# Optimization experiments

Measured on AMD Instinct MI355X. Metric: run time of the kernel, lower is better.

Reference implementation:

```python
import jax, jax.numpy as jnp
import numpy as np

GROUPS = 1024
K_N = 32
FEAT_DIM = 64
EPS = 1e-05


def farthest_point_sample(xyz, npoint):
    # xyz: [B, N, 3] -> centroids [B, npoint] int32
    # Original torch code starts from a random point; we use index 0 for determinism.
    B, N, _ = xyz.shape

    def step(carry, _):
        distance, farthest = carry
        centroid = jnp.take_along_axis(xyz, farthest[:, None, None], axis=1)  # [B,1,3]
        dist = jnp.sum((xyz - centroid) ** 2, axis=-1)  # [B,N]
        distance = jnp.minimum(distance, dist)
        new_far = jnp.argmax(distance, axis=-1).astype(jnp.int32)
        return (distance, new_far), farthest

    init = (jnp.full((B, N), 1e10, dtype=xyz.dtype), jnp.zeros((B,), jnp.int32))
    _, cents = jax.lax.scan(step, init, None, length=npoint)
    return cents.T  # [B, npoint]


def index_points(points, idx):
    # points: [B, N, C]; idx: [B, ...] -> [B, ..., C]
    B = points.shape[0]
    bidx = jnp.arange(B).reshape((B,) + (1,) * (idx.ndim - 1))
    return points[bidx, idx]


def square_distance(src, dst):
    # src [B,S,C], dst [B,N,C] -> [B,S,N]
    d = -2.0 * jnp.einsum('bsc,bnc->bsn', src, dst)
    d = d + jnp.sum(src ** 2, -1)[:, :, None]
    d = d + jnp.sum(dst ** 2, -1)[:, None, :]
    return d


def setup_inputs() -> dict:
    key = jax.random.key(0)
    k1, k2 = jax.random.split(key)
    xyz = jax.random.normal(k1, (8, 3, 4096), dtype=jnp.float32)
    feats = jax.random.normal(k2, (8, FEAT_DIM, 4096), dtype=jnp.float32)
    affine_alpha_p = jnp.ones((1, 1, 1, FEAT_DIM), jnp.float32)
    affine_beta_p = jnp.zeros((1, 1, 1, FEAT_DIM), jnp.float32)
    return {"xyz": xyz, "feats": feats,
            "affine_alpha_p": affine_alpha_p, "affine_beta_p": affine_beta_p}


def reference(xyz, feats, affine_alpha_p, affine_beta_p):
    xyz = jnp.transpose(xyz, (0, 2, 1))      # [B,N,3]
    feats = jnp.transpose(feats, (0, 2, 1))  # [B,N,D]
    B, N, _ = xyz.shape
    S, k = GROUPS, K_N

    fps_idx = farthest_point_sample(xyz, S)          # [B,S]
    new_xyz = index_points(xyz, fps_idx)             # [B,S,3]
    new_feats = index_points(feats, fps_idx)         # [B,S,D]

    sqr = square_distance(new_xyz, xyz)              # [B,S,N]
    _, idx = jax.lax.top_k(-sqr, k)                  # smallest-k -> [B,S,k]
    grouped = index_points(feats, idx)               # [B,S,k,D]

    mean = new_feats[:, :, None, :]                  # [B,S,1,D]
    diff = grouped - mean
    # torch.std over flattened per-batch, unbiased (ddof=1)
    std = jnp.std(diff.reshape(B, -1), axis=-1, ddof=1)[:, None, None, None]
    grouped = diff / (std + EPS)
    grouped = affine_alpha_p * grouped + affine_beta_p

    point_feats = jnp.concatenate(
        [grouped, grouped - new_feats[:, :, None, :]], axis=-1)  # [B,S,k,2D]

    new_feats_out = jnp.transpose(new_feats, (0, 2, 1))          # [B,D,S]
    new_xyz_out = jnp.transpose(new_xyz, (0, 2, 1))              # [B,3,S]
    point_feats_out = jnp.transpose(point_feats, (0, 3, 1, 2))   # [B,2D,S,k]
    return (new_xyz_out, new_feats_out, point_feats_out)
```

## Files before the change

kernel.cpp:

```cpp
#include <hip/hip_runtime.h>

#define NPTS 4096
#define NSAMP 1024
#define KNN_K 32
#define FDIM 64
#define EPSF 1e-5f

typedef float v2f __attribute__((ext_vector_type(2)));

#define DPP_FMAX(CTRL)                                                           \
  {                                                                              \
    int _o = __builtin_amdgcn_update_dpp(0, __float_as_int(wv), CTRL, 0xf, 0xf,  \
                                         true);                                  \
    wv = fmaxf(wv, __int_as_float(_o));                                          \
  }

#define DPP_MAX64(CTRL)                                                          \
  {                                                                              \
    unsigned _olo = (unsigned)__builtin_amdgcn_update_dpp(0, (int)klo, CTRL,     \
                                                          0xf, 0xf, true);       \
    unsigned _ohi = (unsigned)__builtin_amdgcn_update_dpp(0, (int)khi, CTRL,     \
                                                          0xf, 0xf, true);       \
    unsigned long long _ok = ((unsigned long long)_ohi << 32) | _olo;            \
    unsigned long long _ck = ((unsigned long long)khi << 32) | klo;              \
    if (_ok > _ck) { klo = _olo; khi = _ohi; }                                   \
  }

__global__ __launch_bounds__(512) void fps_kernel(const float* __restrict__ xyz,
                                                  int* __restrict__ fps_idx,
                                                  float* __restrict__ sqnorm) {
#pragma clang fp contract(off)
  __shared__ float4 pts[NPTS];
  __shared__ unsigned long long skeys[2][8];
  __shared__ int fpsb[NSAMP];
  const int b = blockIdx.x, t = threadIdx.x;
  const int lane = t & 63, w = t >> 6;
  const float* xb = xyz + (size_t)b * 3 * NPTS;
  v2f px[4], py[4], pz[4];
  float dist[8];
#pragma unroll
  for (int j = 0; j < 4; ++j) {
    int p0 = (2 * j) * 512 + t, p1 = (2 * j + 1) * 512 + t;
    float x0 = xb[p0], y0 = xb[NPTS + p0], z0 = xb[2 * NPTS + p0];
    float x1 = xb[p1], y1 = xb[NPTS + p1], z1 = xb[2 * NPTS + p1];
    float sq0 = __fadd_rn(__fadd_rn(__fmul_rn(x0, x0), __fmul_rn(y0, y0)),
                          __fmul_rn(z0, z0));
    float sq1 = __fadd_rn(__fadd_rn(__fmul_rn(x1, x1), __fmul_rn(y1, y1)),
                          __fmul_rn(z1, z1));
    pts[p0] = make_float4(x0, y0, z0, sq0);
    pts[p1] = make_float4(x1, y1, z1, sq1);
    sqnorm[b * NPTS + p0] = sq0;
    sqnorm[b * NPTS + p1] = sq1;
    px[j].x = x0; px[j].y = x1;
    py[j].x = y0; py[j].y = y1;
    pz[j].x = z0; pz[j].y = z1;
    dist[2 * j] = 1e10f;
    dist[2 * j + 1] = 1e10f;
  }
  if (t == 0) fpsb[0] = 0;
  __syncthreads();
  float4 c = pts[0];
  for (int it = 1; it < NSAMP; ++it) {
    v2f vcx, vcy, vcz;
    vcx.x = c.x; vcx.y = c.x;
    vcy.x = c.y; vcy.y = c.y;
    vcz.x = c.z; vcz.y = c.z;
#pragma unroll
    for (int j = 0; j < 4; ++j) {
      v2f dx = px[j] - vcx;
      v2f dy = py[j] - vcy;
      v2f dz = pz[j] - vcz;
      v2f dd = (dx * dx + dy * dy) + dz * dz;
      dist[2 * j] = fminf(dist[2 * j], dd.x);
      dist[2 * j + 1] = fminf(dist[2 * j + 1], dd.y);
    }
    float m0 = fmaxf(dist[0], dist[1]), m1 = fmaxf(dist[2], dist[3]);
    float m2 = fmaxf(dist[4], dist[5]), m3 = fmaxf(dist[6], dist[7]);
    float wv = fmaxf(fmaxf(m0, m1), fmaxf(m2, m3));
    DPP_FMAX(0x111)
    DPP_FMAX(0x112)
    DPP_FMAX(0x114)
    DPP_FMAX(0x118)
    DPP_FMAX(0x142)
    DPP_FMAX(0x143)
    unsigned wvb = (unsigned)__builtin_amdgcn_readlane(__float_as_int(wv), 63);
    float wvf = __uint_as_float(wvb);
    int kk = 0, found = 0;
    unsigned long long mm = 0ull;
#pragma unroll
    for (int k = 0; k < 8; ++k) {
      unsigned long long m = __ballot(dist[k] == wvf);
      if (!found && m != 0ull) { kk = k; mm = m; found = 1; }
    }
    int fl = __ffsll(mm) - 1;
    unsigned idx = (unsigned)(kk * 512 + (w << 6) + fl);
    unsigned klo = (wvb << 12) | (4095u - idx);
    unsigned khi = wvb >> 20;
    const int buf = it & 1;
    if (lane == 63) skeys[buf][w] = ((unsigned long long)khi << 32) | klo;
    __syncthreads();
    unsigned long long kk2 = skeys[buf][lane & 7];
    klo = (unsigned)kk2;
    khi = (unsigned)(kk2 >> 32);
    DPP_MAX64(0x111)
    DPP_MAX64(0x112)
    DPP_MAX64(0x114)
    unsigned flo = (unsigned)__builtin_amdgcn_readlane((int)klo, 7);
    int far = 4095 - (int)(flo & 0xfffu);
    if (t == 0) fpsb[it] = far;
    c = pts[far];
  }
  __syncthreads();
#pragma unroll
  for (int k = 0; k < 2; ++k)
    fps_idx[b * NSAMP + k * 512 + t] = fpsb[k * 512 + t];
}

__global__ __launch_bounds__(256) void gather_feats_kernel(const float* __restrict__ feats,
                                                           const int* __restrict__ fps,
                                                           float* __restrict__ out1,
                                                           float* __restrict__ nf) {
  int i = blockIdx.x * 256 + threadIdx.x;
  int s = i & 1023, c = (i >> 10) & 63, b = i >> 16;
  int p = fps[(b << 10) + s];
  float v = feats[((size_t)(b * 64 + c)) * NPTS + p];
  out1[(b * 64 + c) * 1024 + s] = v;
  nf[(((b << 10) + s) << 6) + c] = v;
}

__global__ __launch_bounds__(256) void gather_xyz_kernel(const float* __restrict__ xyz,
                                                         const float* __restrict__ sqnorm,
                                                         const int* __restrict__ fps,
                                                         float* __restrict__ out0,
                                                         float4* __restrict__ nx4) {
  int i = blockIdx.x * 256 + threadIdx.x;
  int b = i >> 10, s = i & 1023;
  int p = fps[i];
  const float* xb = xyz + (size_t)b * 3 * NPTS;
  float x = xb[p], y = xb[NPTS + p], z = xb[2 * NPTS + p];
  nx4[i] = make_float4(x, y, z, sqnorm[b * NPTS + p]);
  out0[(b * 3 + 0) * 1024 + s] = x;
  out0[(b * 3 + 1) * 1024 + s] = y;
  out0[(b * 3 + 2) * 1024 + s] = z;
}

__device__ __forceinline__ unsigned long long mk_key(float xn, float yn, float zn,
                                                     float sq, float cx, float cy,
                                                     float cz, float src2, int n) {
  float dot = __fmaf_rn(zn, cz, __fmaf_rn(yn, cy, __fmul_rn(xn, cx)));
  float d = __fadd_rn(__fadd_rn(__fmul_rn(-2.0f, dot), src2), sq);
  unsigned mb = __float_as_uint(d);
  mb = (mb & 0x80000000u) ? ~mb : (mb | 0x80000000u);
  return ((unsigned long long)mb << 32) | (unsigned)n;
}

__global__ __launch_bounds__(256, 2) void knn_kernel(const float* __restrict__ xyz,
                                                     const float* __restrict__ sqnorm,
                                                     const float4* __restrict__ nx4,
                                                     int* __restrict__ knn) {
  const int lane = threadIdx.x & 63;
  const int w = threadIdx.x >> 6;
  const int row = blockIdx.x * 4 + w;
  const int b = row >> 10;
  const float4 c4 = nx4[row];
  const float cx = c4.x, cy = c4.y, cz = c4.z, src2 = c4.w;
  const float4* x4 = (const float4*)(xyz + (size_t)b * 3 * NPTS);
  const float4* y4 = (const float4*)(xyz + (size_t)b * 3 * NPTS + NPTS);
  const float4* z4 = (const float4*)(xyz + (size_t)b * 3 * NPTS + 2 * NPTS);
  const float4* s4 = (const float4*)(sqnorm + (size_t)b * NPTS);
  unsigned long long key[64];
#pragma unroll
  for (int jj = 0; jj < 16; ++jj) {
    int vi = jj * 64 + lane;
    float4 xv = x4[vi], yv = y4[vi], zv = z4[vi], sv = s4[vi];
    int n0 = vi * 4;
    key[jj * 4 + 0] = mk_key(xv.x, yv.x, zv.x, sv.x, cx, cy, cz, src2, n0);
    key[jj * 4 + 1] = mk_key(xv.y, yv.y, zv.y, sv.y, cx, cy, cz, src2, n0 + 1);
    key[jj * 4 + 2] = mk_key(xv.z, yv.z, zv.z, sv.z, cx, cy, cz, src2, n0 + 2);
    key[jj * 4 + 3] = mk_key(xv.w, yv.w, zv.w, sv.w, cx, cy, cz, src2, n0 + 3);
  }
  unsigned long long last = 0ull;
  const int out_base = row * KNN_K;
#pragma unroll 1
  for (int r = 0; r < KNN_K; ++r) {
    unsigned long long cur = ~0ull;
#pragma unroll
    for (int j = 0; j < 64; ++j) {
      unsigned long long k = key[j];
      if (k > last && k < cur) cur = k;
    }
#pragma unroll
    for (int off = 32; off > 0; off >>= 1) {
      unsigned long long o = __shfl_xor(cur, off);
      cur = (o < cur) ? o : cur;
    }
    last = cur;
    if (lane == r) knn[out_base + r] = (int)(unsigned)(cur & 0xffffffffull);
  }
}

__global__ __launch_bounds__(256) void stats_kernel(const float* __restrict__ feats,
                                                    const float* __restrict__ nf,
                                                    const int* __restrict__ knn,
                                                    double* __restrict__ stats) {
  const int b = blockIdx.x >> 5;
  const int chunk = blockIdx.x & 31;
  const int base = chunk * 65536;
  double sm = 0.0, sq = 0.0;
  for (int i = 0; i < 256; ++i) {
    int e = base + i * 256 + threadIdx.x;
    int c = e >> 15;
    int sk = e & 32767;
    int s = sk >> 5, j = sk & 31;
    int p = knn[((((b << 10) + s)) << 5) + j];
    float f = feats[((size_t)(b * 64 + c)) * NPTS + p];
    float m = nf[(((b << 10) + s) << 6) + c];
    double d = (double)__fsub_rn(f, m);
    sm += d;
    sq += d * d;
  }
#pragma unroll
  for (int off = 32; off > 0; off >>= 1) {
    sm += __shfl_down(sm, off);
    sq += __shfl_down(sq, off);
  }
  __shared__ double red[8];
  int w = threadIdx.x >> 6;
  if ((threadIdx.x & 63) == 0) { red[w * 2] = sm; red[w * 2 + 1] = sq; }
  __syncthreads();
  if (threadIdx.x == 0) {
    atomicAdd(&stats[b * 2 + 0], red[0] + red[2] + red[4] + red[6]);
    atomicAdd(&stats[b * 2 + 1], red[1] + red[3] + red[5] + red[7]);
  }
}

__global__ __launch_bounds__(256) void out_kernel(const float* __restrict__ feats,
                                                  const float* __restrict__ nf,
                                                  const int* __restrict__ knn,
                                                  const double* __restrict__ stats,
                                                  const float* __restrict__ alpha,
                                                  const float* __restrict__ beta,
                                                  float* __restrict__ out2) {
  const int plane = blockIdx.x;
  const int b = plane >> 6, c = plane & 63;
  const int sk = blockIdx.y * 256 + threadIdx.x;
  const int s = sk >> 5, j = sk & 31;
  const double n = 2097152.0;
  double sm = stats[b * 2], sqs = stats[b * 2 + 1];
  double var = (sqs - sm * sm / n) / (n - 1.0);
  float stdf = (float)sqrt(var);
  float denom = stdf + EPSF;
  int p = knn[((((b << 10) + s)) << 5) + j];
  float f = feats[((size_t)(b * 64 + c)) * NPTS + p];
  float m = nf[(((b << 10) + s) << 6) + c];
  float diff = __fsub_rn(f, m);
  float g = alpha[c] * (diff / denom) + beta[c];
  size_t o1 = (((size_t)(b * 128 + c) << 10) + (size_t)s) * 32 + j;
  size_t o2 = (((size_t)(b * 128 + 64 + c) << 10) + (size_t)s) * 32 + j;
  out2[o1] = g;
  out2[o2] = g - m;
}

extern "C" void kernel_launch(void* const* d_in, const int* in_sizes, int n_in,
                              void* d_out, int out_size, void* d_ws, size_t ws_size,
                              hipStream_t stream) {
  (void)in_sizes; (void)n_in; (void)out_size; (void)ws_size;
  const float* xyz   = (const float*)d_in[0];
  const float* feats = (const float*)d_in[1];
  const float* alpha = (const float*)d_in[2];
  const float* beta  = (const float*)d_in[3];
  float* out  = (float*)d_out;
  float* out0 = out;
  float* out1 = out + 24576;
  float* out2 = out + 24576 + 524288;

  char* ws = (char*)d_ws;
  int*    fps   = (int*)ws;
  float*  sqn   = (float*)(ws + 32768);
  float4* nx4   = (float4*)(ws + 163840);
  float*  nf    = (float*)(ws + 294912);
  int*    knn   = (int*)(ws + 2392064);
  double* stats = (double*)(ws + 3440640);

  hipMemsetAsync(stats, 0, 128, stream);
  fps_kernel<<<8, 512, 0, stream>>>(xyz, fps, sqn);
  gather_feats_kernel<<<2048, 256, 0, stream>>>(feats, fps, out1, nf);
  gather_xyz_kernel<<<32, 256, 0, stream>>>(xyz, sqn, fps, out0, nx4);
  knn_kernel<<<2048, 256, 0, stream>>>(xyz, sqn, nx4, knn);
  stats_kernel<<<256, 256, 0, stream>>>(feats, nf, knn, stats);
  out_kernel<<<dim3(512, 128), 256, 0, stream>>>(feats, nf, knn, stats, alpha, beta, out2);
}
```

Before: 1.171 ms.

## Use single-pass packed argmax in FPS and fuse xyz gather into it

The FPS loop now finds the per-thread best (distance, index) locally and reduces a packed 64-bit key across the wavefront with DPP. This replaces the earlier float-max DPP reduction followed by a readlane and eight ballots used to recover the index, shortening the serial per-iteration critical path. The separate gather_xyz kernel is removed, and FPS writes out0 and nx4 directly from its shared-memory point table, saving a launch. Each DPP step now moves two 32-bit halves instead of one, and fps_idx is written from thread 0 inside the loop.

```diff
diff --git a/kernel.cpp b/kernel.cpp
--- a/kernel.cpp
+++ b/kernel.cpp
@@ -7,13 +7,6 @@
 #define EPSF 1e-5f
 
 typedef float v2f __attribute__((ext_vector_type(2)));
-
-#define DPP_FMAX(CTRL)                                                           \
-  {                                                                              \
-    int _o = __builtin_amdgcn_update_dpp(0, __float_as_int(wv), CTRL, 0xf, 0xf,  \
-                                         true);                                  \
-    wv = fmaxf(wv, __int_as_float(_o));                                          \
-  }
 
 #define DPP_MAX64(CTRL)                                                          \
   {                                                                              \
@@ -28,7 +21,9 @@
 
 __global__ __launch_bounds__(512) void fps_kernel(const float* __restrict__ xyz,
                                                   int* __restrict__ fps_idx,
-                                                  float* __restrict__ sqnorm) {
+                                                  float* __restrict__ sqnorm,
+                                                  float* __restrict__ out0,
+                                                  float4* __restrict__ nx4) {
 #pragma clang fp contract(off)
   __shared__ float4 pts[NPTS];
   __shared__ unsigned long long skeys[2][8];
@@ -36,8 +31,7 @@
   const int b = blockIdx.x, t = threadIdx.x;
   const int lane = t & 63, w = t >> 6;
   const float* xb = xyz + (size_t)b * 3 * NPTS;
-  v2f px[4], py[4], pz[4];
-  float dist[8];
+  v2f px[4], py[4], pz[4], dst[4];
 #pragma unroll
   for (int j = 0; j < 4; ++j) {
     int p0 = (2 * j) * 512 + t, p1 = (2 * j + 1) * 512 + t;
@@ -54,10 +48,10 @@
     px[j].x = x0; px[j].y = x1;
     py[j].x = y0; py[j].y = y1;
     pz[j].x = z0; pz[j].y = z1;
-    dist[2 * j] = 1e10f;
-    dist[2 * j + 1] = 1e10f;
-  }
-  if (t == 0) fpsb[0] = 0;
+    dst[j].x = 1e10f;
+    dst[j].y = 1e10f;
+  }
+  if (t == 0) { fps_idx[b * NSAMP] = 0; fpsb[0] = 0; }
   __syncthreads();
   float4 c = pts[0];
   for (int it = 1; it < NSAMP; ++it) {
@@ -71,49 +65,51 @@
       v2f dy = py[j] - vcy;
       v2f dz = pz[j] - vcz;
       v2f dd = (dx * dx + dy * dy) + dz * dz;
-      dist[2 * j] = fminf(dist[2 * j], dd.x);
-      dist[2 * j + 1] = fminf(dist[2 * j + 1], dd.y);
-    }
-    float m0 = fmaxf(dist[0], dist[1]), m1 = fmaxf(dist[2], dist[3]);
-    float m2 = fmaxf(dist[4], dist[5]), m3 = fmaxf(dist[6], dist[7]);
-    float wv = fmaxf(fmaxf(m0, m1), fmaxf(m2, m3));
-    DPP_FMAX(0x111)
-    DPP_FMAX(0x112)
-    DPP_FMAX(0x114)
-    DPP_FMAX(0x118)
-    DPP_FMAX(0x142)
-    DPP_FMAX(0x143)
-    unsigned wvb = (unsigned)__builtin_amdgcn_readlane(__float_as_int(wv), 63);
-    float wvf = __uint_as_float(wvb);
-    int kk = 0, found = 0;
-    unsigned long long mm = 0ull;
+      dst[j].x = fminf(dst[j].x, dd.x);
+      dst[j].y = fminf(dst[j].y, dd.y);
+    }
+    float bv = -1.0f;
+    int bi = 0;
 #pragma unroll
     for (int k = 0; k < 8; ++k) {
-      unsigned long long m = __ballot(dist[k] == wvf);
-      if (!found && m != 0ull) { kk = k; mm = m; found = 1; }
-    }
-    int fl = __ffsll(mm) - 1;
-    unsigned idx = (unsigned)(kk * 512 + (w << 6) + fl);
-    unsigned klo = (wvb << 12) | (4095u - idx);
-    unsigned khi = wvb >> 20;
+      float nd = (k & 1) ? dst[k >> 1].y : dst[k >> 1].x;
+      int n = k * 512 + t;
+      if (nd > bv) { bv = nd; bi = n; }
+    }
+    unsigned bvb = __float_as_uint(bv);
+    unsigned klo = (bvb << 12) | (unsigned)(4095 - bi);
+    unsigned khi = bvb >> 20;
+    DPP_MAX64(0x111)
+    DPP_MAX64(0x112)
+    DPP_MAX64(0x114)
+    DPP_MAX64(0x118)
+    DPP_MAX64(0x142)
+    DPP_MAX64(0x143)
     const int buf = it & 1;
     if (lane == 63) skeys[buf][w] = ((unsigned long long)khi << 32) | klo;
     __syncthreads();
-    unsigned long long kk2 = skeys[buf][lane & 7];
-    klo = (unsigned)kk2;
-    khi = (unsigned)(kk2 >> 32);
+    unsigned long long kk = skeys[buf][lane & 7];
+    klo = (unsigned)kk;
+    khi = (unsigned)(kk >> 32);
     DPP_MAX64(0x111)
     DPP_MAX64(0x112)
     DPP_MAX64(0x114)
     unsigned flo = (unsigned)__builtin_amdgcn_readlane((int)klo, 7);
     int far = 4095 - (int)(flo & 0xfffu);
-    if (t == 0) fpsb[it] = far;
+    if (t == 0) { fps_idx[b * NSAMP + it] = far; fpsb[it] = far; }
     c = pts[far];
   }
   __syncthreads();
 #pragma unroll
-  for (int k = 0; k < 2; ++k)
-    fps_idx[b * NSAMP + k * 512 + t] = fpsb[k * 512 + t];
+  for (int k = 0; k < 2; ++k) {
+    int s = k * 512 + t;
+    int p = fpsb[s];
+    float4 q = pts[p];
+    out0[(b * 3 + 0) * 1024 + s] = q.x;
+    out0[(b * 3 + 1) * 1024 + s] = q.y;
+    out0[(b * 3 + 2) * 1024 + s] = q.z;
+    nx4[b * 1024 + s] = q;
+  }
 }
 
 __global__ __launch_bounds__(256) void gather_feats_kernel(const float* __restrict__ feats,
@@ -126,22 +122,6 @@
   float v = feats[((size_t)(b * 64 + c)) * NPTS + p];
   out1[(b * 64 + c) * 1024 + s] = v;
   nf[(((b << 10) + s) << 6) + c] = v;
-}
-
-__global__ __launch_bounds__(256) void gather_xyz_kernel(const float* __restrict__ xyz,
-                                                         const float* __restrict__ sqnorm,
-                                                         const int* __restrict__ fps,
-                                                         float* __restrict__ out0,
-                                                         float4* __restrict__ nx4) {
-  int i = blockIdx.x * 256 + threadIdx.x;
-  int b = i >> 10, s = i & 1023;
-  int p = fps[i];
-  const float* xb = xyz + (size_t)b * 3 * NPTS;
-  float x = xb[p], y = xb[NPTS + p], z = xb[2 * NPTS + p];
-  nx4[i] = make_float4(x, y, z, sqnorm[b * NPTS + p]);
-  out0[(b * 3 + 0) * 1024 + s] = x;
-  out0[(b * 3 + 1) * 1024 + s] = y;
-  out0[(b * 3 + 2) * 1024 + s] = z;
 }
 
 __device__ __forceinline__ unsigned long long mk_key(float xn, float yn, float zn,
@@ -283,9 +263,8 @@
   double* stats = (double*)(ws + 3440640);
 
   hipMemsetAsync(stats, 0, 128, stream);
-  fps_kernel<<<8, 512, 0, stream>>>(xyz, fps, sqn);
+  fps_kernel<<<8, 512, 0, stream>>>(xyz, fps, sqn, out0, nx4);
   gather_feats_kernel<<<2048, 256, 0, stream>>>(feats, fps, out1, nf);
-  gather_xyz_kernel<<<32, 256, 0, stream>>>(xyz, sqn, fps, out0, nx4);
   knn_kernel<<<2048, 256, 0, stream>>>(xyz, sqn, nx4, knn);
   stats_kernel<<<256, 256, 0, stream>>>(feats, nf, knn, stats);
   out_kernel<<<dim3(512, 128), 256, 0, stream>>>(feats, nf, knn, stats, alpha, beta, out2);
```

Result: faster. 977.0 us (-16.6%).
